# Performance work log

Hardware: AMD Instinct MI355X
Metric: run time of the kernel (lower is better)

The kernel has to match this reference:

```python
import jax, jax.numpy as jnp
import numpy as np

# ---- config (mirrors cfg / init kwargs) ----
FEAT_STRIDE = 16
IM_DIMS = (1024, 1024)          # (height, width)
ANCHOR_SCALES = (8, 16, 32)
ANCHOR_RATIOS = (0.5, 1.0, 2.0)
PRE_NMS_TOPN = 6000             # eval mode (cfg_key=1)
POST_NMS_TOPN = 300
NMS_THRESH = 0.7
MIN_SIZE = 16


def _generate_base_anchors(base_size=16, ratios=ANCHOR_RATIOS, scales=ANCHOR_SCALES):
    """py-faster-rcnn generate_anchors, in numpy (static)."""
    def mk(ws, hs, xc, yc):
        return np.stack([xc - 0.5 * (ws - 1), yc - 0.5 * (hs - 1),
                         xc + 0.5 * (ws - 1), yc + 0.5 * (hs - 1)], axis=1)
    base = np.array([0, 0, base_size - 1, base_size - 1], dtype=np.float64)
    w = base[2] - base[0] + 1; h = base[3] - base[1] + 1
    xc = base[0] + 0.5 * (w - 1); yc = base[1] + 0.5 * (h - 1)
    # ratio enum
    size = w * h
    ws = np.round(np.sqrt(size / np.array(ratios)))
    hs = np.round(ws * np.array(ratios))
    ratio_anchors = mk(ws, hs, xc, yc)
    # scale enum
    out = []
    for a in ratio_anchors:
        aw = a[2] - a[0] + 1; ah = a[3] - a[1] + 1
        axc = a[0] + 0.5 * (aw - 1); ayc = a[1] + 0.5 * (ah - 1)
        out.append(mk(aw * np.array(scales), ah * np.array(scales), axc, ayc))
    return np.concatenate(out, axis=0).astype(np.float32)  # [A,4]


def _all_anchors(H, W):
    base = _generate_base_anchors()                       # [A,4]
    sx = np.arange(W) * FEAT_STRIDE
    sy = np.arange(H) * FEAT_STRIDE
    sx, sy = np.meshgrid(sx, sy)
    shifts = np.stack([sx.ravel(), sy.ravel(), sx.ravel(), sy.ravel()], axis=1)  # [H*W,4]
    anchors = shifts[:, None, :].astype(np.float32) + base[None, :, :]
    return anchors.reshape(-1, 4)                         # [H*W*A, 4]


def setup_inputs() -> dict:
    key = jax.random.key(0)
    k1, k2 = jax.random.split(key)
    H, W, A = 64, 64, 9
    rpn_cls_score = jax.random.normal(k1, (1, H, W, 2 * A), dtype=jnp.float32)
    rpn_bbox_pred = jax.random.normal(k2, (1, H, W, 4 * A), dtype=jnp.float32)
    return {"rpn_cls_score": rpn_cls_score, "rpn_bbox_pred": rpn_bbox_pred}


def _proposals(rpn_cls_score, rpn_bbox_pred):
    _, H, W, C2 = rpn_cls_score.shape
    A = C2 // 2
    # rpn_softmax: per-anchor 2-way softmax, foreground prob
    scores = jax.nn.softmax(rpn_cls_score.reshape(H, W, A, 2), axis=-1)[..., 1].reshape(-1)  # [N]
    deltas = rpn_bbox_pred.reshape(-1, 4)                  # [N,4]
    anchors = jnp.asarray(_all_anchors(H, W))              # [N,4]
    # bbox_transform_inv
    aw = anchors[:, 2] - anchors[:, 0] + 1.0
    ah = anchors[:, 3] - anchors[:, 1] + 1.0
    axc = anchors[:, 0] + 0.5 * aw
    ayc = anchors[:, 1] + 0.5 * ah
    dx, dy, dw, dh = deltas[:, 0], deltas[:, 1], deltas[:, 2], deltas[:, 3]
    pxc = dx * aw + axc; pyc = dy * ah + ayc
    pw = jnp.exp(dw) * aw; ph = jnp.exp(dh) * ah
    x1 = pxc - 0.5 * pw; y1 = pyc - 0.5 * ph
    x2 = pxc + 0.5 * pw; y2 = pyc + 0.5 * ph
    # clip to image
    im_h, im_w = IM_DIMS
    x1 = jnp.clip(x1, 0.0, im_w - 1.0); x2 = jnp.clip(x2, 0.0, im_w - 1.0)
    y1 = jnp.clip(y1, 0.0, im_h - 1.0); y2 = jnp.clip(y2, 0.0, im_h - 1.0)
    boxes = jnp.stack([x1, y1, x2, y2], axis=1)            # [N,4]
    # filter too-small boxes by masking their score
    valid = ((x2 - x1 + 1.0) >= MIN_SIZE) & ((y2 - y1 + 1.0) >= MIN_SIZE)
    scores = jnp.where(valid, scores, -jnp.inf)
    return boxes, scores


def _nms_keep(boxes, K):
    """Greedy NMS keep-mask over score-descending boxes [K,4]."""
    x1, y1, x2, y2 = boxes[:, 0], boxes[:, 1], boxes[:, 2], boxes[:, 3]
    areas = (x2 - x1 + 1.0) * (y2 - y1 + 1.0)
    ix1 = jnp.maximum(x1[:, None], x1[None, :])
    iy1 = jnp.maximum(y1[:, None], y1[None, :])
    ix2 = jnp.minimum(x2[:, None], x2[None, :])
    iy2 = jnp.minimum(y2[:, None], y2[None, :])
    iw = jnp.maximum(ix2 - ix1 + 1.0, 0.0)
    ih = jnp.maximum(iy2 - iy1 + 1.0, 0.0)
    inter = iw * ih
    iou = inter / (areas[:, None] + areas[None, :] - inter)  # [K,K]
    idxs = jnp.arange(K)
    def body(i, keep):
        sup = keep[i] & (iou[i] > NMS_THRESH) & (idxs > i)
        return keep & ~sup
    return jax.lax.fori_loop(0, K, body, jnp.ones((K,), bool))


def reference(rpn_cls_score, rpn_bbox_pred):
    boxes, scores = _proposals(rpn_cls_score, rpn_bbox_pred)
    K = min(PRE_NMS_TOPN, scores.shape[0])
    top_scores, order = jax.lax.top_k(scores, K)           # score-descending
    top_boxes = boxes[order]                               # [K,4]
    keep = _nms_keep(top_boxes, K)
    sel_scores = jnp.where(keep, top_scores, -jnp.inf)
    _, idx = jax.lax.top_k(sel_scores, POST_NMS_TOPN)      # kept, in score order
    out_boxes = top_boxes[idx]                             # [post,4]
    blob = jnp.concatenate([jnp.zeros((POST_NMS_TOPN, 1), out_boxes.dtype), out_boxes], axis=1)
    return blob                                            # [post,5] (batch_idx, x1,y1,x2,y2)
```

## Files before the change

### kernel.cpp

```cpp
#include <hip/hip_runtime.h>
#include <stdint.h>

typedef unsigned long long u64;
typedef unsigned int u32;

#define N_ANCH 36864
#define WGRID 64
#define A_PER 9
#define KTOP 6000
#define NOUT 300
#define NBIN 5120
#define NCHK 94
#define NJ   6016
#define INF_BIN 0
#define PCAP 6

#define BARRIER_LDS() do {                                   \
    asm volatile("s_waitcnt lgkmcnt(0)" ::: "memory");       \
    __builtin_amdgcn_s_barrier();                            \
    asm volatile("" ::: "memory");                           \
} while (0)

__constant__ float c_ax1[9] = {-84.f,-176.f,-360.f,-56.f,-120.f,-248.f,-36.f,-80.f,-168.f};
__constant__ float c_ay1[9] = {-40.f,-88.f,-184.f,-56.f,-120.f,-248.f,-80.f,-168.f,-344.f};
__constant__ float c_aw[9]  = {184.f,368.f,736.f,128.f,256.f,512.f,88.f,176.f,352.f};
__constant__ float c_ah[9]  = {96.f,192.f,384.f,128.f,256.f,512.f,176.f,352.f,704.f};

__device__ __forceinline__ u32 binof(u32 u) {
    if (u < 0x80000000u) return 0u;
    if (u < 0xBF000000u) return 1u + ((u - 0x80000000u) >> 22);
    return 256u + ((u - 0xBF000000u) >> 11);
}

__global__ __launch_bounds__(256) void proposal_kernel(const float* __restrict__ cls,
                                                       const float* __restrict__ dlt,
                                                       u64* __restrict__ keys,
                                                       float4* __restrict__ boxes,
                                                       u32* __restrict__ hist) {
    __shared__ u32 lh[NBIN];
    const int t = threadIdx.x;
    for (int b = t; b < NBIN; b += 256) lh[b] = 0;
    __syncthreads();

    int i = blockIdx.x * 256 + t;
    int a  = i % A_PER;
    int hw = i / A_PER;
    int wx = hw % WGRID;
    int hy = hw / WGRID;

    float2 lp = *(const float2*)(cls + hw * 18 + 2 * a);
    float l0 = lp.x, l1 = lp.y;
    float m  = fmaxf(l0, l1);
    float e0 = expf(l0 - m), e1 = expf(l1 - m);
    float s  = e1 / (e0 + e1);

    float4 dd = *(const float4*)(dlt + hw * 36 + 4 * a);
    float dx = dd.x, dy = dd.y, dw = dd.z, dh = dd.w;
    float aw = c_aw[a], ah = c_ah[a];
    float axc = (c_ax1[a] + 16.f * (float)wx) + 0.5f * aw;
    float ayc = (c_ay1[a] + 16.f * (float)hy) + 0.5f * ah;

    float pxc = dx * aw + axc;
    float pyc = dy * ah + ayc;
    float pw  = expf(dw) * aw;
    float ph  = expf(dh) * ah;
    float x1 = pxc - 0.5f * pw, y1 = pyc - 0.5f * ph;
    float x2 = pxc + 0.5f * pw, y2 = pyc + 0.5f * ph;
    x1 = fminf(fmaxf(x1, 0.f), 1023.f);
    x2 = fminf(fmaxf(x2, 0.f), 1023.f);
    y1 = fminf(fmaxf(y1, 0.f), 1023.f);
    y2 = fminf(fmaxf(y2, 0.f), 1023.f);
    bool valid = ((x2 - x1 + 1.f) >= 16.f) && ((y2 - y1 + 1.f) >= 16.f);
    float sc = valid ? s : -__builtin_huge_valf();

    u32 sb  = __float_as_uint(sc);
    u32 ord = (sb & 0x80000000u) ? ~sb : (sb | 0x80000000u);
    u64 key = ((u64)ord << 32) | (u32)(~(u32)i);
    keys[i]  = key;
    boxes[i] = make_float4(x1, y1, x2, y2);

    u64 infb = __ballot(!valid);
    if (valid) {
        atomicAdd(&lh[binof(ord)], 1u);
    } else {
        int lane = t & 63;
        if (lane == __builtin_ctzll(infb))
            atomicAdd(&lh[INF_BIN], (u32)__popcll(infb));
    }
    __syncthreads();
    for (int b = t; b < NBIN; b += 256) {
        u32 v = lh[b];
        if (v) atomicAdd(&hist[b], v);
    }
}

__global__ __launch_bounds__(1024) void scan_kernel(const u32* __restrict__ hist,
                                                    u32* __restrict__ binStart,
                                                    u32* __restrict__ gEV) {
    __shared__ u32 wsum[16];
    const int t = threadIdx.x;
    const int lane = t & 63;
    const int v = t >> 6;
    if (t == 0) gEV[1] = KTOP;
    int hi = NBIN - 1 - 5 * t;
    u32 cnt[5];
    u32 sum = 0;
#pragma unroll
    for (int k = 0; k < 5; ++k) { cnt[k] = hist[hi - k]; sum += cnt[k]; }
    u32 s = sum;
#pragma unroll
    for (int d = 1; d < 64; d <<= 1) {
        u32 x = __shfl_up(s, d, 64);
        if (lane >= d) s += x;
    }
    if (lane == 63) wsum[v] = s;
    __syncthreads();
    u32 base = 0;
#pragma unroll
    for (int q = 0; q < 16; ++q) {
        u32 x = wsum[q];
        if (q < v) base += x;
    }
    u32 run = base + s - sum;
#pragma unroll
    for (int k = 0; k < 5; ++k) {
        int b = hi - k;
        binStart[b] = run;
        u32 end = run + cnt[k];
        if (run < KTOP && end >= KTOP) gEV[0] = end;
        run = end;
    }
}

__global__ void scatter_kernel(const u64* __restrict__ keys,
                               const u32* __restrict__ binStart,
                               u32* __restrict__ cursor,
                               u64* __restrict__ scat) {
    int i = blockIdx.x * blockDim.x + threadIdx.x;
    if (i >= N_ANCH) return;
    u64 k = keys[i];
    u32 b = binof((u32)(k >> 32));
    u32 s = binStart[b];
    if (s < KTOP) {
        u32 p = s + atomicAdd(&cursor[b], 1u);
        scat[p] = k;
    }
}

__global__ void rank_kernel(const u64* __restrict__ scat,
                            const u32* __restrict__ binStart,
                            const u32* __restrict__ hist,
                            const float4* __restrict__ boxes,
                            const u32* __restrict__ gEV,
                            float4* __restrict__ topBoxes,
                            int* __restrict__ gV) {
    int i = blockIdx.x * blockDim.x + threadIdx.x;
    u32 E = gEV[0];
    if (i >= (int)E) return;
    u64 k = scat[i];
    u32 b = binof((u32)(k >> 32));
    u32 s = binStart[b], c = hist[b];
    u32 r = s;
    for (u32 j = s; j < s + c; ++j) r += (scat[j] > k) ? 1u : 0u;
    if (r < KTOP) {
        int idx = (int)(~(u32)k);
        topBoxes[r] = boxes[idx];
        if (!(k >> 63)) atomicMin(gV, (int)r);
    }
}

__device__ __forceinline__ bool iou_gt(float4 a, float areaA, float4 b, float areaB) {
    float ix1 = fmaxf(a.x, b.x), iy1 = fmaxf(a.y, b.y);
    float ix2 = fminf(a.z, b.z), iy2 = fminf(a.w, b.w);
    float iw = fmaxf(ix2 - ix1 + 1.0f, 0.0f);
    float ih = fmaxf(iy2 - iy1 + 1.0f, 0.0f);
    float inter = iw * ih;
    float iou = inter / (areaA + areaB - inter);
    return iou > 0.7f;
}

__global__ __launch_bounds__(256) void maskT_kernel(const float4* __restrict__ topBoxes,
                                                    const u32* __restrict__ gEV,
                                                    u64* __restrict__ S) {
    const int V = (int)gEV[1];
    const int nch = (V + 63) >> 6;
    const int jc = blockIdx.x;
    const int w0 = blockIdx.y * 4;
    if (jc >= nch || w0 > jc) return;
    __shared__ float4 cb[256];
    __shared__ float  ca[256];
    const int t = threadIdx.x;
    const int lane = t & 63;
    {
        int ci = w0 * 64 + t;
        float4 b = (ci < V) ? topBoxes[ci] : make_float4(0.f, 0.f, -8.f, -8.f);
        cb[t] = b;
        ca[t] = (b.z - b.x + 1.f) * (b.w - b.y + 1.f);
    }
    __syncthreads();
    const int w = w0 + (t >> 6);
    if (w > jc || w >= nch) return;
    const int j = jc * 64 + lane;
    float4 bj = (j < V) ? topBoxes[j] : make_float4(0.f, 0.f, -8.f, -8.f);
    float aj = (bj.z - bj.x + 1.f) * (bj.w - bj.y + 1.f);
    const int s0 = (t >> 6) * 64;
    u64 m = 0;
#pragma unroll 4
    for (int b = 0; b < 64; ++b)
        if (iou_gt(bj, aj, cb[s0 + b], ca[s0 + b])) m |= (1ull << b);
    if (w == jc) m &= ((1ull << lane) - 1ull);
    S[(u64)w * NJ + j] = m;
}

__global__ __launch_bounds__(1024) void nms_out_kernel(const float4* __restrict__ topBoxes,
                                                       const u32* __restrict__ gEV,
                                                       const u64* __restrict__ S,
                                                       float* __restrict__ out) {
    __shared__ u64 keepw[NCHK];
    __shared__ u64 supw[2][16];
    __shared__ u32 wsum[16];
    const int t = threadIdx.x;
    const int lane = t & 63;
    const int v = t >> 6;
    if (t < NCHK) keepw[t] = 0;
    const int V = (int)gEV[1];
    const int nch = (V + 63) >> 6;

    u64 kw[PCAP], pendE[PCAP], pendO[PCAP];
#pragma unroll
    for (int k = 0; k < PCAP; ++k) { kw[k] = 0; pendE[k] = 0; pendO[k] = 0; }
    u64 dtE = 0, dtO = 0;
#pragma unroll
    for (int k = 0; k < PCAP; ++k) {
        int w = v + 16 * k;
        if (w < 1 && 1 < nch) pendO[k] = S[(u64)w * NJ + 64 + lane];
    }
    dtE = S[lane];
    if (nch > 1) dtO = S[(u64)NJ + 64 + lane];
    int nkept = 0;

    for (int c = 0; c < nch; ++c) {
        const int par = c & 1;
        u64 acc = 0;
        if (par) {
#pragma unroll
            for (int k = 0; k < PCAP; ++k) { int w = v + 16 * k; if (w < c) acc |= pendO[k] & kw[k]; }
        } else {
#pragma unroll
            for (int k = 0; k < PCAP; ++k) { int w = v + 16 * k; if (w < c) acc |= pendE[k] & kw[k]; }
        }
        u64 bal = __ballot(acc != 0ull);
        if (lane == 0) supw[par][v] = bal;
        const int cn = c + 2;
        if (cn < nch) {
            const u64* Sc = S + (u64)cn * 64 + lane;
            if (par) {
#pragma unroll
                for (int k = 0; k < PCAP; ++k) { int w = v + 16 * k; if (w < cn) pendO[k] = Sc[(u64)w * NJ]; }
            } else {
#pragma unroll
                for (int k = 0; k < PCAP; ++k) { int w = v + 16 * k; if (w < cn) pendE[k] = Sc[(u64)w * NJ]; }
            }
        }
        BARRIER_LDS();
        u64 sup = 0;
#pragma unroll
        for (int q = 0; q < 16; ++q) sup |= supw[par][q];
        int rem = V - c * 64;
        u64 aliveM = (rem >= 64) ? ~0ull : ((1ull << rem) - 1ull);
        u64 cand = ~sup & aliveM;
        u64 dT = par ? dtO : dtE;
        u64 kb = 0;
        while (cand) {
            int b = __builtin_ctzll(cand);
            kb |= (1ull << b);
            cand &= ~(1ull << b);
            cand &= ~__ballot(((dT >> b) & 1ull) != 0ull);
        }
        if (t == 0) keepw[c] = kb;
        if (cn < nch) {
            u64 dload = S[(u64)cn * NJ + (u64)cn * 64 + lane];
            if (par) dtO = dload; else dtE = dload;
        }
#pragma unroll
        for (int k = 0; k < PCAP; ++k)
            if (v + 16 * k == c) kw[k] = kb;
        nkept += __popcll(kb);
        if (nkept >= NOUT) break;
    }
    __syncthreads();

    const int per = 6;
    int r0 = t * per;
    int r1 = min(r0 + per, KTOP);
    u32 cnt = 0;
    for (int r = r0; r < r1; ++r)
        cnt += (u32)((keepw[r >> 6] >> (r & 63)) & 1ull);
    u32 s = cnt;
#pragma unroll
    for (int d = 1; d < 64; d <<= 1) {
        u32 x = __shfl_up(s, d, 64);
        if (lane >= d) s += x;
    }
    if (lane == 63) wsum[v] = s;
    __syncthreads();
    u32 base = 0;
    u32 total = 0;
#pragma unroll
    for (int q = 0; q < 16; ++q) {
        u32 x = wsum[q];
        if (q < v) base += x;
        total += x;
    }
    const int n1 = min((int)total, NOUT);
    int kp = (int)(base + s - cnt);
    for (int r = r0; r < r1; ++r) {
        int kept = (int)((keepw[r >> 6] >> (r & 63)) & 1ull);
        int pos = kept ? kp : (n1 + r - kp);
        if (pos < NOUT) {
            float4 b = topBoxes[r];
            out[pos * 5 + 0] = 0.f;
            out[pos * 5 + 1] = b.x;
            out[pos * 5 + 2] = b.y;
            out[pos * 5 + 3] = b.z;
            out[pos * 5 + 4] = b.w;
        }
        kp += kept;
    }
}

extern "C" void kernel_launch(void* const* d_in, const int* in_sizes, int n_in,
                              void* d_out, int out_size, void* d_ws, size_t ws_size,
                              hipStream_t stream) {
    const float* cls = (const float*)d_in[0];
    const float* dlt = (const float*)d_in[1];
    float* out = (float*)d_out;
    char* ws = (char*)d_ws;
    u64*    keys     = (u64*)   (ws);
    u64*    scat     = (u64*)   (ws + 294912);
    float4* boxes    = (float4*)(ws + 589824);
    float4* topBoxes = (float4*)(ws + 1179648);
    u32*    hist     = (u32*)   (ws + 1275648);
    u32*    cursor   = (u32*)   (ws + 1296128);
    u32*    binStart = (u32*)   (ws + 1316608);
    u32*    gEV      = (u32*)   (ws + 1337088);
    u64*    S        = (u64*)   (ws + 1337344);

    hipMemsetAsync(hist, 0, 2 * NBIN * sizeof(u32), stream);
    proposal_kernel<<<144, 256, 0, stream>>>(cls, dlt, keys, boxes, hist);
    scan_kernel<<<1, 1024, 0, stream>>>(hist, binStart, gEV);
    scatter_kernel<<<(N_ANCH + 255) / 256, 256, 0, stream>>>(keys, binStart, cursor, scat);
    rank_kernel<<<(N_ANCH + 255) / 256, 256, 0, stream>>>(scat, binStart, hist, boxes, gEV,
                                                          topBoxes, (int*)&gEV[1]);
    maskT_kernel<<<dim3(NCHK, (NCHK + 3) / 4), 256, 0, stream>>>(topBoxes, gEV, S);
    nms_out_kernel<<<1, 1024, 0, stream>>>(topBoxes, gEV, S, out);
}
```

Before: 131.3 us.

## Process NMS chunks in pairs with compacted kept-chunk slots and LDS diagonals

The serial NMS keep-scan now handles two 64-box chunks per barrier step instead of one, which roughly halves the number of block-wide barriers. The diagonal and cross-diagonal suppression blocks are preloaded into shared memory up front. Only chunks that actually kept boxes get register slots, with an LDS spill list for overflow, so fewer suppression-matrix rows are loaded per step. In exchange it adds a second serial ballot loop per step, a larger LDS footprint, and extra complexity in the slot bookkeeping.

```diff
diff --git a/kernel.cpp b/kernel.cpp
--- a/kernel.cpp
+++ b/kernel.cpp
@@ -11,9 +11,11 @@
 #define NOUT 300
 #define NBIN 5120
 #define NCHK 94
+#define NCH2 47
 #define NJ   6016
 #define INF_BIN 0
-#define PCAP 6
+#define SLOTS 4
+#define SPILLCAP 32
 
 #define BARRIER_LDS() do {                                   \
     asm volatile("s_waitcnt lgkmcnt(0)" ::: "memory");       \
@@ -216,76 +218,122 @@
                                                        const u32* __restrict__ gEV,
                                                        const u64* __restrict__ S,
                                                        float* __restrict__ out) {
+    __shared__ u64 dA[NCH2][64];
+    __shared__ u64 dAB[NCH2][64];
+    __shared__ u64 dB[NCH2][64];
     __shared__ u64 keepw[NCHK];
-    __shared__ u64 supw[2][16];
+    __shared__ u64 supw[2][32];
+    __shared__ u64 spillK[SPILLCAP];
+    __shared__ u32 spillW[SPILLCAP];
     __shared__ u32 wsum[16];
     const int t = threadIdx.x;
     const int lane = t & 63;
     const int v = t >> 6;
-    if (t < NCHK) keepw[t] = 0;
     const int V = (int)gEV[1];
     const int nch = (V + 63) >> 6;
-
-    u64 kw[PCAP], pendE[PCAP], pendO[PCAP];
-#pragma unroll
-    for (int k = 0; k < PCAP; ++k) { kw[k] = 0; pendE[k] = 0; pendO[k] = 0; }
-    u64 dtE = 0, dtO = 0;
-#pragma unroll
-    for (int k = 0; k < PCAP; ++k) {
-        int w = v + 16 * k;
-        if (w < 1 && 1 < nch) pendO[k] = S[(u64)w * NJ + 64 + lane];
-    }
-    dtE = S[lane];
-    if (nch > 1) dtO = S[(u64)NJ + 64 + lane];
-    int nkept = 0;
-
-    for (int c = 0; c < nch; ++c) {
-        const int par = c & 1;
-        u64 acc = 0;
-        if (par) {
-#pragma unroll
-            for (int k = 0; k < PCAP; ++k) { int w = v + 16 * k; if (w < c) acc |= pendO[k] & kw[k]; }
-        } else {
-#pragma unroll
-            for (int k = 0; k < PCAP; ++k) { int w = v + 16 * k; if (w < c) acc |= pendE[k] & kw[k]; }
-        }
-        u64 bal = __ballot(acc != 0ull);
-        if (lane == 0) supw[par][v] = bal;
-        const int cn = c + 2;
-        if (cn < nch) {
-            const u64* Sc = S + (u64)cn * 64 + lane;
-            if (par) {
-#pragma unroll
-                for (int k = 0; k < PCAP; ++k) { int w = v + 16 * k; if (w < cn) pendO[k] = Sc[(u64)w * NJ]; }
-            } else {
-#pragma unroll
-                for (int k = 0; k < PCAP; ++k) { int w = v + 16 * k; if (w < cn) pendE[k] = Sc[(u64)w * NJ]; }
+    const int nr  = (nch + 1) >> 1;
+    if (t < NCHK) keepw[t] = 0;
+    for (int idx = t; idx < nr * 64; idx += 1024) {
+        int r = idx >> 6, l = idx & 63;
+        dA[r][l]  = S[(u64)(2 * r) * NJ + 128 * r + l];
+        dAB[r][l] = S[(u64)(2 * r) * NJ + 128 * r + 64 + l];
+        dB[r][l]  = S[(u64)(2 * r + 1) * NJ + 128 * r + 64 + l];
+    }
+    __syncthreads();
+
+    u64 kwS[SLOTS], pA[SLOTS], pB[SLOTS], aofs[SLOTS];
+#pragma unroll
+    for (int k = 0; k < SLOTS; ++k) { kwS[k] = 0; pA[k] = 0; pB[k] = 0; aofs[k] = 0; }
+    int nslot = 0, nspill = 0, nkept = 0;
+
+    for (int r = 0; r < nr; ++r) {
+        const int par = r & 1;
+        u64 accA = 0, accB = 0;
+#pragma unroll
+        for (int k = 0; k < SLOTS; ++k) {
+            if (nslot > 16 * k + v) { accA |= pA[k] & kwS[k]; accB |= pB[k] & kwS[k]; }
+        }
+        for (int s = 0; s < nspill; ++s) {
+            u64 kk = spillK[s];
+            const u64* row = S + (u64)spillW[s] * NJ + 128 * r + lane;
+            accA |= row[0] & kk; accB |= row[64] & kk;
+        }
+        u64 bA = __ballot(accA != 0ull), bB = __ballot(accB != 0ull);
+        if (lane == 0) { supw[par][v] = bA; supw[par][16 + v] = bB; }
+        if (r + 1 < nr) {
+            u64 ofsn = (u64)(128 * (r + 1)) + lane;
+#pragma unroll
+            for (int k = 0; k < SLOTS; ++k)
+                if (nslot > 16 * k + v) { pA[k] = S[aofs[k] + ofsn]; pB[k] = S[aofs[k] + ofsn + 64]; }
+        }
+        BARRIER_LDS();
+        u64 x = supw[par][lane & 31];
+#pragma unroll
+        for (int m = 1; m < 16; m <<= 1) x |= __shfl_xor(x, m, 64);
+        u64 rwA = __shfl(x, 0, 64);
+        u64 rwB = __shfl(x, 16, 64);
+        int remA = V - 128 * r;
+        int remB = remA - 64;
+        u64 aliveA = (remA >= 64) ? ~0ull : ((remA <= 0) ? 0ull : ((1ull << remA) - 1ull));
+        u64 aliveB = (remB >= 64) ? ~0ull : ((remB <= 0) ? 0ull : ((1ull << remB) - 1ull));
+        u64 dAl = dA[r][lane], dABl = dAB[r][lane], dBl = dB[r][lane];
+        u64 candA = ~rwA & aliveA, kbA = 0;
+        while (candA) {
+            int b = __builtin_ctzll(candA);
+            kbA |= (1ull << b);
+            candA &= ~(1ull << b);
+            candA &= ~__ballot(((dAl >> b) & 1ull) != 0ull);
+        }
+        u64 supAB = __ballot((dABl & kbA) != 0ull);
+        u64 candB = ~(rwB | supAB) & aliveB, kbB = 0;
+        while (candB) {
+            int b = __builtin_ctzll(candB);
+            kbB |= (1ull << b);
+            candB &= ~(1ull << b);
+            candB &= ~__ballot(((dBl >> b) & 1ull) != 0ull);
+        }
+        if (t == 0) { keepw[2 * r] = kbA; if (2 * r + 1 < nch) keepw[2 * r + 1] = kbB; }
+        bool sadd = false;
+        if (kbA) {
+            int so = nslot & 15, si = nslot >> 4;
+            if (si < SLOTS) {
+                if (v == so) {
+#pragma unroll
+                    for (int k = 0; k < SLOTS; ++k) if (k == si) {
+                        kwS[k] = kbA; aofs[k] = (u64)(2 * r) * NJ;
+                        if (r + 1 < nr) {
+                            u64 o = (u64)(128 * (r + 1)) + lane;
+                            pA[k] = S[aofs[k] + o]; pB[k] = S[aofs[k] + o + 64];
+                        }
+                    }
+                }
+                ++nslot;
+            } else if (nspill < SPILLCAP) {
+                if (v == 15 && lane == 0) { spillW[nspill] = 2 * r; spillK[nspill] = kbA; }
+                ++nspill; sadd = true;
             }
         }
-        BARRIER_LDS();
-        u64 sup = 0;
-#pragma unroll
-        for (int q = 0; q < 16; ++q) sup |= supw[par][q];
-        int rem = V - c * 64;
-        u64 aliveM = (rem >= 64) ? ~0ull : ((1ull << rem) - 1ull);
-        u64 cand = ~sup & aliveM;
-        u64 dT = par ? dtO : dtE;
-        u64 kb = 0;
-        while (cand) {
-            int b = __builtin_ctzll(cand);
-            kb |= (1ull << b);
-            cand &= ~(1ull << b);
-            cand &= ~__ballot(((dT >> b) & 1ull) != 0ull);
-        }
-        if (t == 0) keepw[c] = kb;
-        if (cn < nch) {
-            u64 dload = S[(u64)cn * NJ + (u64)cn * 64 + lane];
-            if (par) dtO = dload; else dtE = dload;
-        }
-#pragma unroll
-        for (int k = 0; k < PCAP; ++k)
-            if (v + 16 * k == c) kw[k] = kb;
-        nkept += __popcll(kb);
+        if (kbB) {
+            int so = nslot & 15, si = nslot >> 4;
+            if (si < SLOTS) {
+                if (v == so) {
+#pragma unroll
+                    for (int k = 0; k < SLOTS; ++k) if (k == si) {
+                        kwS[k] = kbB; aofs[k] = (u64)(2 * r + 1) * NJ;
+                        if (r + 1 < nr) {
+                            u64 o = (u64)(128 * (r + 1)) + lane;
+                            pA[k] = S[aofs[k] + o]; pB[k] = S[aofs[k] + o + 64];
+                        }
+                    }
+                }
+                ++nslot;
+            } else if (nspill < SPILLCAP) {
+                if (v == 15 && lane == 0) { spillW[nspill] = 2 * r + 1; spillK[nspill] = kbB; }
+                ++nspill; sadd = true;
+            }
+        }
+        if (sadd) BARRIER_LDS();
+        nkept += __popcll(kbA) + __popcll(kbB);
         if (nkept >= NOUT) break;
     }
     __syncthreads();
```

Result: no change. 130.2 us (-0.8%).
